# Performance work log

Hardware: AMD Instinct MI355X
Metric: run time of the kernel (lower is better)

The kernel has to match this reference:

```python
import jax, jax.numpy as jnp
import numpy as np

# init_kwargs: zs (sorted list of supported atomic numbers)
ZS = jnp.array([0, 1, 6, 7, 8, 11, 13, 14, 16, 17, 26, 29, 47, 78, 79, 83], dtype=jnp.float32)

N_ATOMS = 8_000_000


def setup_inputs() -> dict:
    key = jax.random.key(0)
    # integer-valued atomic numbers in [0, 83); float dtype so gradients exist
    z = jax.random.randint(key, (N_ATOMS,), 0, 83).astype(jnp.float32)
    return {"atomic_numbers": z}


def reference(atomic_numbers):
    K = ZS.shape[0]
    # first index j with ZS[j] >= z (vectorized replacement of the python loop)
    j = jnp.clip(jnp.searchsorted(ZS, atomic_numbers, side="left"), 0, K - 1)
    z_hi = ZS[j]
    exact = z_hi == atomic_numbers           # one-hot branch: z in zs
    j_lo = jnp.clip(j - 1, 0, K - 1)
    z_lo = ZS[j_lo]
    denom = jnp.where(exact, 1.0, z_hi - z_lo)   # safe divide when j_lo == j
    w_hi = jnp.where(exact, 1.0, (atomic_numbers - z_lo) / denom)
    w_lo = jnp.where(exact, 0.0, (z_hi - atomic_numbers) / denom)
    # fused one-hot/interpolation write: [N, K]
    encoded = (w_hi[:, None] * jax.nn.one_hot(j, K, dtype=jnp.float32)
               + w_lo[:, None] * jax.nn.one_hot(j_lo, K, dtype=jnp.float32))
    return encoded
```

## Files before the change

### kernel.cpp

```cpp
#include <hip/hip_runtime.h>


#define K_TAB 16
#define N_Z   83
#define CHUNK 1024
#define BLOCK 256
#define INNER (CHUNK * 4 / BLOCK)

typedef float v4f __attribute__((ext_vector_type(4)));

__device__ __forceinline__ void lds_only_barrier() {
    __asm__ volatile("s_waitcnt lgkmcnt(0)" ::: "memory");
    __builtin_amdgcn_s_barrier();
    __builtin_amdgcn_sched_barrier(0);
}

__device__ __forceinline__ v4f load_chunk_z(const float* __restrict__ z_in,
                                            int c, int tid, int n_atoms) {
    const int a0 = c * CHUNK + tid * 4;
    v4f r = {0.f, 0.f, 0.f, 0.f};
    if (a0 + 3 < n_atoms) {
        r = *reinterpret_cast<const v4f*>(&z_in[a0]);
    } else {
#pragma unroll
        for (int e = 0; e < 4; ++e)
            if (a0 + e < n_atoms) r[e] = z_in[a0 + e];
    }
    return r;
}

__global__ __launch_bounds__(BLOCK) void node_encode_kernel(
    const float* __restrict__ z_in,
    float* __restrict__ out,
    int n_atoms, int n_chunks)
{
    __shared__ float lut[N_Z][K_TAB];
    __shared__ float zbuf[2][CHUNK];

    const int tid = threadIdx.x;

    constexpr float tab[K_TAB] = {0.f, 1.f, 6.f, 7.f, 8.f, 11.f, 13.f, 14.f,
                                  16.f, 17.f, 26.f, 29.f, 47.f, 78.f, 79.f, 83.f};
    if (tid < N_Z) {
        const float zf = (float)tid;
        int j = 0;
        float zlo = tab[0];
        float zhi = tab[K_TAB - 1];
#pragma unroll
        for (int k = 0; k < K_TAB; ++k) {
            const bool lt = (tab[k] < zf);
            j += lt ? 1 : 0;
            zlo = lt ? tab[k] : zlo;
        }
#pragma unroll
        for (int k = K_TAB - 2; k >= 0; --k) {
            zhi = (tab[k] >= zf) ? tab[k] : zhi;
        }
        const bool exact = (zhi == zf);
        const float denom = exact ? 1.f : (zhi - zlo);
        const float inv   = 1.f / denom;
        const float whi   = exact ? 1.f : (zf - zlo) * inv;
        const float wlo   = exact ? 0.f : (zhi - zf) * inv;
        int jl = j - (exact ? 0 : 1);
        if (jl < 0) jl = 0;
#pragma unroll
        for (int c = 0; c < K_TAB; ++c) {
            lut[tid][c] = (c == j ? whi : 0.f) + (c == jl ? wlo : 0.f);
        }
    }

    v4f* __restrict__ out4 = reinterpret_cast<v4f*>(out);
    const int total4 = n_atoms * 4;

    int c = blockIdx.x;
    if (c < n_chunks) {
        const v4f z0 = load_chunk_z(z_in, c, tid, n_atoms);
        *reinterpret_cast<v4f*>(&zbuf[0][tid * 4]) = z0;
    }
    lds_only_barrier();

    int p = 0;
    for (; c < n_chunks; c += gridDim.x, ++p) {
        const int cn = c + gridDim.x;
        const bool haveN = (cn < n_chunks);
        v4f zregN = {0.f, 0.f, 0.f, 0.f};
        if (haveN) zregN = load_chunk_z(z_in, cn, tid, n_atoms);

        const float* __restrict__ zb = zbuf[p & 1];
        const int base4 = c * (CHUNK * 4);
        if (base4 + CHUNK * 4 <= total4) {
#pragma unroll
            for (int k = 0; k < INNER; ++k) {
                const int u  = k * BLOCK + tid;
                const int zi = (int)zb[u >> 2];
                const v4f v  = *reinterpret_cast<const v4f*>(&lut[zi][(u & 3) << 2]);
                out4[base4 + u] = v;
            }
        } else {
            for (int k = 0; k < INNER; ++k) {
                const int u = k * BLOCK + tid;
                const int g = base4 + u;
                if (g < total4) {
                    const int zi = (int)zb[u >> 2];
                    out4[g] = *reinterpret_cast<const v4f*>(&lut[zi][(u & 3) << 2]);
                }
            }
        }

        if (haveN) {
            *reinterpret_cast<v4f*>(&zbuf[(p + 1) & 1][tid * 4]) = zregN;
        }
        lds_only_barrier();
    }
}

extern "C" void kernel_launch(void* const* d_in, const int* in_sizes, int n_in,
                              void* d_out, int out_size, void* d_ws, size_t ws_size,
                              hipStream_t stream) {
    const float* z = (const float*)d_in[0];
    float* out = (float*)d_out;
    const int n_atoms = in_sizes[0];

    const int n_chunks = (n_atoms + CHUNK - 1) / CHUNK;
    const int phases   = 4;
    int grid = (n_chunks + phases - 1) / phases;
    if (grid > 2048) grid = 2048;

    node_encode_kernel<<<grid, BLOCK, 0, stream>>>(z, out, n_atoms, n_chunks);
}
```

Measured before the change: 110.2 us.

## Assign contiguous chunk ranges to a fixed 512-block grid with larger chunks

```diff
diff --git a/kernel.cpp b/kernel.cpp
--- a/kernel.cpp
+++ b/kernel.cpp
@@ -3,11 +3,14 @@
 
 #define K_TAB 16
 #define N_Z   83
-#define CHUNK 1024
+#define CHUNK 2048
 #define BLOCK 256
 #define INNER (CHUNK * 4 / BLOCK)
+#define GRID  512
 
 typedef float v4f __attribute__((ext_vector_type(4)));
+
+struct zpair { v4f a, b; };
 
 __device__ __forceinline__ void lds_only_barrier() {
     __asm__ volatile("s_waitcnt lgkmcnt(0)" ::: "memory");
@@ -15,16 +18,22 @@
     __builtin_amdgcn_sched_barrier(0);
 }
 
-__device__ __forceinline__ v4f load_chunk_z(const float* __restrict__ z_in,
-                                            int c, int tid, int n_atoms) {
-    const int a0 = c * CHUNK + tid * 4;
-    v4f r = {0.f, 0.f, 0.f, 0.f};
-    if (a0 + 3 < n_atoms) {
-        r = *reinterpret_cast<const v4f*>(&z_in[a0]);
+__device__ __forceinline__ zpair load_chunk_z(const float* __restrict__ z_in,
+                                              int c, int tid, int n_atoms) {
+    const long a0 = (long)c * CHUNK + tid * 8;
+    zpair r;
+    r.a = (v4f){0.f, 0.f, 0.f, 0.f};
+    r.b = (v4f){0.f, 0.f, 0.f, 0.f};
+    if (a0 + 7 < n_atoms) {
+        r.a = *reinterpret_cast<const v4f*>(&z_in[a0]);
+        r.b = *reinterpret_cast<const v4f*>(&z_in[a0 + 4]);
     } else {
 #pragma unroll
         for (int e = 0; e < 4; ++e)
-            if (a0 + e < n_atoms) r[e] = z_in[a0 + e];
+            if (a0 + e < n_atoms) r.a[e] = z_in[a0 + e];
+#pragma unroll
+        for (int e = 0; e < 4; ++e)
+            if (a0 + 4 + e < n_atoms) r.b[e] = z_in[a0 + 4 + e];
     }
     return r;
 }
@@ -69,25 +78,32 @@
         }
     }
 
+    const int b = blockIdx.x;
+    const int q = n_chunks / GRID;
+    const int r = n_chunks % GRID;
+    const int c_begin = b * q + (b < r ? b : r);
+    const int c_end   = c_begin + q + (b < r ? 1 : 0);
+
     v4f* __restrict__ out4 = reinterpret_cast<v4f*>(out);
-    const int total4 = n_atoms * 4;
+    const long total4 = (long)n_atoms * 4;
 
-    int c = blockIdx.x;
-    if (c < n_chunks) {
-        const v4f z0 = load_chunk_z(z_in, c, tid, n_atoms);
-        *reinterpret_cast<v4f*>(&zbuf[0][tid * 4]) = z0;
+    if (c_begin < c_end) {
+        const zpair z0 = load_chunk_z(z_in, c_begin, tid, n_atoms);
+        *reinterpret_cast<v4f*>(&zbuf[0][tid * 8])     = z0.a;
+        *reinterpret_cast<v4f*>(&zbuf[0][tid * 8 + 4]) = z0.b;
     }
     lds_only_barrier();
 
     int p = 0;
-    for (; c < n_chunks; c += gridDim.x, ++p) {
-        const int cn = c + gridDim.x;
-        const bool haveN = (cn < n_chunks);
-        v4f zregN = {0.f, 0.f, 0.f, 0.f};
-        if (haveN) zregN = load_chunk_z(z_in, cn, tid, n_atoms);
+    for (int c = c_begin; c < c_end; ++c, ++p) {
+        const bool haveN = (c + 1 < c_end);
+        zpair zregN;
+        zregN.a = (v4f){0.f, 0.f, 0.f, 0.f};
+        zregN.b = (v4f){0.f, 0.f, 0.f, 0.f};
+        if (haveN) zregN = load_chunk_z(z_in, c + 1, tid, n_atoms);
 
         const float* __restrict__ zb = zbuf[p & 1];
-        const int base4 = c * (CHUNK * 4);
+        const long base4 = (long)c * (CHUNK * 4);
         if (base4 + CHUNK * 4 <= total4) {
 #pragma unroll
             for (int k = 0; k < INNER; ++k) {
@@ -99,7 +115,7 @@
         } else {
             for (int k = 0; k < INNER; ++k) {
                 const int u = k * BLOCK + tid;
-                const int g = base4 + u;
+                const long g = base4 + u;
                 if (g < total4) {
                     const int zi = (int)zb[u >> 2];
                     out4[g] = *reinterpret_cast<const v4f*>(&lut[zi][(u & 3) << 2]);
@@ -108,7 +124,8 @@
         }
 
         if (haveN) {
-            *reinterpret_cast<v4f*>(&zbuf[(p + 1) & 1][tid * 4]) = zregN;
+            *reinterpret_cast<v4f*>(&zbuf[(p + 1) & 1][tid * 8])     = zregN.a;
+            *reinterpret_cast<v4f*>(&zbuf[(p + 1) & 1][tid * 8 + 4]) = zregN.b;
         }
         lds_only_barrier();
     }
@@ -122,9 +139,6 @@
     const int n_atoms = in_sizes[0];
 
     const int n_chunks = (n_atoms + CHUNK - 1) / CHUNK;
-    const int phases   = 4;
-    int grid = (n_chunks + phases - 1) / phases;
-    if (grid > 2048) grid = 2048;
 
-    node_encode_kernel<<<grid, BLOCK, 0, stream>>>(z, out, n_atoms, n_chunks);
+    node_encode_kernel<<<GRID, BLOCK, 0, stream>>>(z, out, n_atoms, n_chunks);
 }
```

Result: no change. 111.4 us (+1.1%).
